# Kernel optimization log

Measured on AMD Instinct MI355X. Metric: run time of the kernel, lower is better.

Reference implementation:

```python
import jax, jax.numpy as jnp
import numpy as np

NUM_ITERS = 3
NUM_HEADS = 4
EPS = 1e-8
LN_EPS = 1e-5


def _layernorm(x, w, b):
    mu = jnp.mean(x, axis=-1, keepdims=True)
    var = jnp.mean(jnp.square(x - mu), axis=-1, keepdims=True)
    return (x - mu) * jax.lax.rsqrt(var + LN_EPS) * w + b


def setup_inputs() -> dict:
    key = jax.random.key(0)
    ks = jax.random.split(key, 12)
    B, K, D, Q, Hm = 64, 4096, 256, 8, 512
    s = 0.02
    return {
        "inputs": jax.random.normal(ks[0], (B, K, D), jnp.float32),
        "slots_init": jax.random.normal(ks[1], (B, Q, D), jnp.float32),
        "Wq": jax.random.normal(ks[2], (D, D), jnp.float32) * s,
        "Wk": jax.random.normal(ks[3], (D, D), jnp.float32) * s,
        "Wv": jax.random.normal(ks[4], (D, D), jnp.float32) * s,
        "ln_in_w": jnp.ones((D,), jnp.float32),
        "ln_in_b": jnp.zeros((D,), jnp.float32),
        "ln_slots_w": jnp.ones((D,), jnp.float32),
        "ln_slots_b": jnp.zeros((D,), jnp.float32),
        "ln_mlp_w": jnp.ones((D,), jnp.float32),
        "ln_mlp_b": jnp.zeros((D,), jnp.float32),
        "gru_Wih": jax.random.normal(ks[5], (3 * D, D), jnp.float32) * s,
        "gru_Whh": jax.random.normal(ks[6], (3 * D, D), jnp.float32) * s,
        "gru_bih": jnp.zeros((3 * D,), jnp.float32),
        "gru_bhh": jnp.zeros((3 * D,), jnp.float32),
        "mlp_W1": jax.random.normal(ks[7], (D, Hm), jnp.float32) * s,
        "mlp_b1": jnp.zeros((Hm,), jnp.float32),
        "mlp_W2": jax.random.normal(ks[8], (Hm, D), jnp.float32) * s,
        "mlp_b2": jnp.zeros((D,), jnp.float32),
    }


def reference(inputs, slots_init, Wq, Wk, Wv, ln_in_w, ln_in_b, ln_slots_w,
              ln_slots_b, ln_mlp_w, ln_mlp_b, gru_Wih, gru_Whh, gru_bih,
              gru_bhh, mlp_W1, mlp_b1, mlp_W2, mlp_b2):
    B, K, D = inputs.shape
    Q = slots_init.shape[1]
    H = NUM_HEADS
    dh = D // H
    scale = dh ** -0.5

    x = _layernorm(inputs, ln_in_w, ln_in_b)
    k = (x @ Wk).reshape(B, K, H, dh).transpose(0, 2, 1, 3) * scale  # [B,H,K,dh]
    v = (x @ Wv).reshape(B, K, H, dh).transpose(0, 2, 1, 3)          # [B,H,K,dh]

    slots = slots_init
    attn = None
    for _ in range(NUM_ITERS):
        slots_prev = slots
        s_n = _layernorm(slots, ln_slots_w, ln_slots_b)
        q = (s_n @ Wq).reshape(B, Q, H, dh).transpose(0, 2, 1, 3)    # [B,H,Q,dh]
        logits = jnp.einsum('bhkd,bhqd->bhkq', k, q)                 # [B,H,K,Q]
        # softmax jointly over (heads, slots) per kv position
        attn = jax.nn.softmax(
            logits.transpose(0, 2, 1, 3).reshape(B, K, H * Q), axis=-1
        ).reshape(B, K, H, Q).transpose(0, 2, 1, 3)                  # [B,H,K,Q]
        attn = attn + EPS
        attn = attn / jnp.sum(attn, axis=2, keepdims=True)           # renorm over K
        updates = jnp.einsum('bhkq,bhkd->bqhd', attn, v).reshape(B, Q, D)

        # GRU cell (PyTorch gate order: r, z, n)
        u = updates.reshape(-1, D)
        h = slots_prev.reshape(-1, D)
        gi = u @ gru_Wih.T + gru_bih
        gh = h @ gru_Whh.T + gru_bhh
        i_r, i_z, i_n = jnp.split(gi, 3, axis=-1)
        h_r, h_z, h_n = jnp.split(gh, 3, axis=-1)
        r = jax.nn.sigmoid(i_r + h_r)
        z = jax.nn.sigmoid(i_z + h_z)
        n = jnp.tanh(i_n + r * h_n)
        slots = ((1.0 - z) * n + z * h).reshape(B, Q, D)

        m = _layernorm(slots, ln_mlp_w, ln_mlp_b)
        slots = slots + jax.nn.relu(m @ mlp_W1 + mlp_b1) @ mlp_W2 + mlp_b2

    return slots, attn.mean(axis=1).transpose(0, 2, 1)  # [B,Q,D], [B,Q,K]
```

## Files before the change

kernel.cpp:

```cpp
#include <hip/hip_runtime.h>

#define B   64
#define KK  4096
#define D   256
#define Q   8
#define H   4
#define DH  64
#define HQ  32
#define HM  512
#define NCH 8
#define CHK 512
#define EPS 1e-8f
#define LNE 1e-5f
#define SCALE 0.125f

typedef short bf16x8 __attribute__((ext_vector_type(8)));
typedef float f32x4 __attribute__((ext_vector_type(4)));

__device__ __forceinline__ float bf2f(unsigned short u) {
    unsigned int x = ((unsigned int)u) << 16;
    float f; __builtin_memcpy(&f, &x, 4); return f;
}
__device__ __forceinline__ unsigned short f2bf(float f) {
    unsigned int x; __builtin_memcpy(&x, &f, 4);
    unsigned int lsb = (x >> 16) & 1u;
    x += 0x7fffu + lsb;
    return (unsigned short)(x >> 16);
}

__device__ __forceinline__ void gload16(const void* g, void* l) {
    __builtin_amdgcn_global_load_lds(
        (const __attribute__((address_space(1))) unsigned int*)g,
        (__attribute__((address_space(3))) unsigned int*)l, 16, 0, 0);
}

__device__ __forceinline__ void stage64x512B(const char* src, size_t row0,
                                             size_t stride, char* lds, int w, int l)
{
#pragma unroll
    for (int i = 0; i < 8; ++i) {
        const int seg = w * 8 + i;
        const int r = seg * 2 + (l >> 5);
        const int off = ((l & 31) * 16) ^ ((r & 7) << 4);
        gload16(src + (row0 + r) * stride + off, lds + seg * 1024);
    }
}

__global__ void k_init(const float* __restrict__ s0, float* __restrict__ slots,
                       unsigned short* __restrict__ slots_bf)
{
    const int i = blockIdx.x * 256 + threadIdx.x;
    const float v = s0[i];
    slots[i] = v; slots_bf[i] = f2bf(v);
}

__global__ __launch_bounds__(256) void k0_wkv(
    const float* __restrict__ Wk, const float* __restrict__ Wv,
    unsigned short* __restrict__ WkvT)
{
    const int c = blockIdx.x, d = threadIdx.x;
    const float v = (c < 256) ? Wk[(size_t)d * 256 + c] * SCALE
                              : Wv[(size_t)d * 256 + (c - 256)];
    WkvT[(size_t)c * 256 + d] = f2bf(v);
}

__global__ void k0_cvt(const float* __restrict__ src, unsigned short* __restrict__ dst)
{
    const int i = blockIdx.x * 256 + threadIdx.x;
    dst[i] = f2bf(src[i]);
}

__global__ void k0_t1(const float* __restrict__ W1, unsigned short* __restrict__ W1T)
{
    const int n = blockIdx.x, d = threadIdx.x;
    W1T[(size_t)n * 256 + d] = f2bf(W1[(size_t)d * 512 + n]);
}

__global__ void k0_t2(const float* __restrict__ W2, unsigned short* __restrict__ W2T)
{
    const int n = blockIdx.x, j = threadIdx.x;
    W2T[(size_t)n * 512 + j]       = f2bf(W2[(size_t)j * 256 + n]);
    W2T[(size_t)n * 512 + 256 + j] = f2bf(W2[(size_t)(256 + j) * 256 + n]);
}

__global__ __launch_bounds__(256) void k1_mfma(
    const float* __restrict__ inp, const unsigned short* __restrict__ WkvT,
    const float* __restrict__ lnw, const float* __restrict__ lnb,
    unsigned short* __restrict__ kbuf, unsigned short* __restrict__ vbufT)
{
    __shared__ char smem[65536];
    char* abase = smem;
    char* bb0 = smem + 32768;
    char* bb1 = smem;
    const int t = threadIdx.x, w = t >> 6, l = t & 63;
    const size_t row0 = (size_t)blockIdx.x * 64;

    float4 xv[16];
#pragma unroll
    for (int i = 0; i < 16; ++i)
        xv[i] = ((const float4*)(inp + (row0 + w * 16 + i) * D))[l];
    const float4 w4 = ((const float4*)lnw)[l];
    const float4 b4 = ((const float4*)lnb)[l];
#pragma unroll
    for (int i = 0; i < 16; ++i) {
        const int r = w * 16 + i;
        float4 x = xv[i];
        float s  = x.x + x.y + x.z + x.w;
        float ss = x.x*x.x + x.y*x.y + x.z*x.z + x.w*x.w;
#pragma unroll
        for (int off = 32; off; off >>= 1) { s += __shfl_xor(s, off); ss += __shfl_xor(ss, off); }
        const float mu = s * (1.f / 256.f);
        const float rs = rsqrtf(ss * (1.f / 256.f) - mu * mu + LNE);
        ushort4 pk;
        pk.x = f2bf((x.x - mu) * rs * w4.x + b4.x);
        pk.y = f2bf((x.y - mu) * rs * w4.y + b4.y);
        pk.z = f2bf((x.z - mu) * rs * w4.z + b4.z);
        pk.w = f2bf((x.w - mu) * rs * w4.w + b4.w);
        *(ushort4*)(abase + r * 512 + ((l * 8) ^ ((r & 7) << 4))) = pk;
    }
    __syncthreads();

    const int arow = w * 16 + (l & 15);
    const char* ap = abase + arow * 512;
    const int asw = (l & 7) << 4;
    bf16x8 af[8];
#pragma unroll
    for (int kk = 0; kk < 8; ++kk)
        af[kk] = *(const bf16x8*)(ap + ((kk * 64 + (l >> 4) * 16) ^ asw));

    stage64x512B((const char*)WkvT, 0, 512, bb0, w, l);
    __syncthreads();

    const f32x4 fz = {0.f, 0.f, 0.f, 0.f};
    for (int n2 = 0; n2 < 8; ++n2) {
        if (n2 < 7)
            stage64x512B((const char*)WkvT, (size_t)(n2 + 1) * 64, 512,
                         ((n2 + 1) & 1) ? bb1 : bb0, w, l);
        const char* bbase = (n2 & 1) ? bb1 : bb0;
        f32x4 acc[4] = {fz, fz, fz, fz};
#pragma unroll
        for (int kk = 0; kk < 8; ++kk) {
            const int koff = kk * 64 + (l >> 4) * 16;
#pragma unroll
            for (int nf = 0; nf < 4; ++nf) {
                const int brow = nf * 16 + (l & 15);
                const bf16x8 bf_ = *(const bf16x8*)(bbase + brow * 512 + (koff ^ ((brow & 7) << 4)));
                acc[nf] = __builtin_amdgcn_mfma_f32_16x16x32_bf16(af[kk], bf_, acc[nf], 0, 0, 0);
            }
        }
        const int c0 = n2 * 64;
        const size_t grow0 = row0 + w * 16 + (l >> 4) * 4;
#pragma unroll
        for (int nf = 0; nf < 4; ++nf) {
            const int c = c0 + nf * 16 + (l & 15);
            if (c < 256) {
#pragma unroll
                for (int reg = 0; reg < 4; ++reg)
                    kbuf[(grow0 + reg) * 256 + c] = f2bf(acc[nf][reg]);
            } else {
                const int cc = c - 256;
                const size_t bb = grow0 >> 12;
                const int kl = (int)(grow0 & 4095);
                ushort4 pk;
                pk.x = f2bf(acc[nf][0]); pk.y = f2bf(acc[nf][1]);
                pk.z = f2bf(acc[nf][2]); pk.w = f2bf(acc[nf][3]);
                *(ushort4*)(vbufT + ((bb * 256 + cc) * KK + kl)) = pk;
            }
        }
        __syncthreads();
    }
}

__global__ __launch_bounds__(256) void k2_qproj(
    const float* __restrict__ slots, const float* __restrict__ Wq,
    const float* __restrict__ lnw, const float* __restrict__ lnb, float* __restrict__ qbuf)
{
    const int row = blockIdx.x, t = threadIdx.x;
    __shared__ float sn[256];
    __shared__ float red[8];
    const float x = slots[(size_t)row * D + t];
    float mu, rs;
    {
        float s = x, ss = x * x;
#pragma unroll
        for (int off = 32; off; off >>= 1) { s += __shfl_xor(s, off); ss += __shfl_xor(ss, off); }
        if ((t & 63) == 0) { red[t >> 6] = s; red[4 + (t >> 6)] = ss; }
        __syncthreads();
        const float S  = red[0] + red[1] + red[2] + red[3];
        const float SS = red[4] + red[5] + red[6] + red[7];
        mu = S * (1.f / 256.f);
        rs = rsqrtf(SS * (1.f / 256.f) - mu * mu + LNE);
    }
    sn[t] = (x - mu) * rs * lnw[t] + lnb[t];
    __syncthreads();
    float acc = 0.f;
    for (int d = 0; d < 256; ++d) acc = fmaf(sn[d], Wq[(size_t)d * 256 + t], acc);
    qbuf[(size_t)row * D + t] = acc;
}

__global__ __launch_bounds__(256) void k_attn(
    const unsigned short* __restrict__ kbuf, const unsigned short* __restrict__ vbufT,
    const float* __restrict__ qbuf, float* __restrict__ updp,
    float* __restrict__ denp, float* __restrict__ pbuf, int write_p)
{
    __shared__ unsigned short ksm[64 * 256];
    __shared__ unsigned short vsm[256 * 64];
    __shared__ unsigned short psm[32 * 64];
    __shared__ float dred[4][32];
    const int t = threadIdx.x, w = t >> 6, l = t & 63;
    const int b = blockIdx.x >> 3, chunk = blockIdx.x & 7;
    const int k0g = chunk * CHK;
    const int n = l & 15, lg = l >> 4;

    auto stage_ks = [&](int tile) {
        const size_t rowg = (size_t)b * KK + k0g + tile * 64;
#pragma unroll
        for (int i = 0; i < 8; ++i) {
            const int seg = w * 8 + i;
            const int r = seg * 2 + (l >> 5);
            const int off = ((l & 31) * 16) ^ ((r & 7) << 4);
            gload16((const char*)kbuf + (rowg + r) * 512 + off, (char*)ksm + seg * 1024);
        }
    };
    auto stage_vs = [&](int tile) {
        const int kk0 = k0g + tile * 64;
#pragma unroll
        for (int i = 0; i < 8; ++i) {
            const int seg = w * 8 + i;
            const int d = seg * 8 + (l >> 3);
            const int off = ((l & 7) * 16) ^ ((d & 7) << 4);
            gload16((const char*)vbufT + (((size_t)b * 256 + d) * KK + kk0) * 2 + off,
                    (char*)vsm + seg * 1024);
        }
    };
    stage_ks(0); stage_vs(0);

    bf16x8 qf[2][2];
#pragma unroll
    for (int p = 0; p < 2; ++p) {
        const int h = p * 2 + (n >> 3);
        const float* qb = qbuf + ((size_t)b * Q + (n & 7)) * D;
#pragma unroll
        for (int j = 0; j < 2; ++j) {
            const int dbase = (h * 2 + j) * 32 + lg * 8;
            short tmp[8];
#pragma unroll
            for (int e = 0; e < 8; ++e) tmp[e] = (short)f2bf(qb[dbase + e]);
            __builtin_memcpy(&qf[p][j], tmp, 16);
        }
    }
    const bf16x8 ZV = {0,0,0,0,0,0,0,0};
    const f32x4 fz = {0.f,0.f,0.f,0.f};
    f32x4 pv[2][4];
#pragma unroll
    for (int mt = 0; mt < 2; ++mt)
#pragma unroll
        for (int nf = 0; nf < 4; ++nf) pv[mt][nf] = fz;
    float den0 = 0.f, den1 = 0.f;

    for (int tile = 0; tile < 8; ++tile) {
        __syncthreads();
        const int arow = w * 16 + n;
        const char* ap = (const char*)ksm + arow * 512;
        const int asw = (arow & 7) << 4;
        f32x4 lac[2] = {fz, fz};
#pragma unroll
        for (int kk = 0; kk < 8; ++kk) {
            const bf16x8 a = *(const bf16x8*)(ap + ((kk * 64 + lg * 16) ^ asw));
            const int p = kk >> 2;
            const bool on = (((kk & 3) >> 1) == (n >> 3));
            const bf16x8 bq = on ? qf[p][kk & 1] : ZV;
            if (p == 0) lac[0] = __builtin_amdgcn_mfma_f32_16x16x32_bf16(a, bq, lac[0], 0, 0, 0);
            else        lac[1] = __builtin_amdgcn_mfma_f32_16x16x32_bf16(a, bq, lac[1], 0, 0, 0);
        }
#pragma unroll
        for (int reg = 0; reg < 4; ++reg) {
            float m = fmaxf(lac[0][reg], lac[1][reg]);
#pragma unroll
            for (int off = 8; off; off >>= 1) m = fmaxf(m, __shfl_xor(m, off));
            const float e0 = __expf(lac[0][reg] - m);
            const float e1 = __expf(lac[1][reg] - m);
            float se = e0 + e1;
#pragma unroll
            for (int off = 8; off; off >>= 1) se += __shfl_xor(se, off);
            const float inv = 1.f / se;
            lac[0][reg] = e0 * inv; lac[1][reg] = e1 * inv;
            den0 += lac[0][reg];    den1 += lac[1][reg];
        }
        const int kb = w * 16 + lg * 4;
        {
            ushort4 p0, p1;
            p0.x = f2bf(lac[0][0]); p0.y = f2bf(lac[0][1]); p0.z = f2bf(lac[0][2]); p0.w = f2bf(lac[0][3]);
            p1.x = f2bf(lac[1][0]); p1.y = f2bf(lac[1][1]); p1.z = f2bf(lac[1][2]); p1.w = f2bf(lac[1][3]);
            *(ushort4*)((char*)psm + n * 128 + ((kb * 2) ^ ((n & 7) << 4))) = p0;
            *(ushort4*)((char*)psm + (16 + n) * 128 + ((kb * 2) ^ ((n & 7) << 4))) = p1;
        }
        if (write_p) {
            float* pp = pbuf + ((size_t)b * KK + k0g + tile * 64 + kb) * HQ;
#pragma unroll
            for (int reg = 0; reg < 4; ++reg) {
                pp[(size_t)reg * HQ + n] = lac[0][reg];
                pp[(size_t)reg * HQ + 16 + n] = lac[1][reg];
            }
        }
        __syncthreads();
        if (tile < 7) stage_ks(tile + 1);
#pragma unroll
        for (int kk = 0; kk < 2; ++kk) {
            const int koff = kk * 64 + lg * 16;
            const bf16x8 a0 = *(const bf16x8*)((char*)psm + n * 128 + (koff ^ ((n & 7) << 4)));
            const bf16x8 a1 = *(const bf16x8*)((char*)psm + (16 + n) * 128 + (koff ^ ((n & 7) << 4)));
#pragma unroll
            for (int nf = 0; nf < 4; ++nf) {
                const int d = w * 64 + nf * 16 + n;
                const bf16x8 bv = *(const bf16x8*)((char*)vsm + d * 128 + (koff ^ ((d & 7) << 4)));
                pv[0][nf] = __builtin_amdgcn_mfma_f32_16x16x32_bf16(a0, bv, pv[0][nf], 0, 0, 0);
                pv[1][nf] = __builtin_amdgcn_mfma_f32_16x16x32_bf16(a1, bv, pv[1][nf], 0, 0, 0);
            }
        }
        __syncthreads();
        if (tile < 7) stage_vs(tile + 1);
    }

    den0 += __shfl_xor(den0, 16); den0 += __shfl_xor(den0, 32);
    den1 += __shfl_xor(den1, 16); den1 += __shfl_xor(den1, 32);
    if (l < 16) { dred[w][l] = den0; dred[w][16 + l] = den1; }
    __syncthreads();
    if (t < 32)
        denp[((size_t)b * NCH + chunk) * HQ + t] =
            dred[0][t] + dred[1][t] + dred[2][t] + dred[3][t];

    if ((lg >> 1) == (w & 1)) {
        const int mt = w >> 1;
#pragma unroll
        for (int nf = 0; nf < 4; ++nf) {
#pragma unroll
            for (int reg = 0; reg < 4; ++reg) {
                const int q = (lg & 1) * 4 + reg;
                updp[(((size_t)b * NCH + chunk) * Q + q) * D + w * 64 + nf * 16 + n] = pv[mt][nf][reg];
            }
        }
    }
}

__global__ __launch_bounds__(256) void k_reduce(
    const float* __restrict__ updp, const float* __restrict__ denp,
    unsigned short* __restrict__ updbf)
{
    const int row = blockIdx.x, t = threadIdx.x;
    const int b = row >> 3, q = row & 7, h = t >> 6;
    float ds = 0.f, us = 0.f;
#pragma unroll
    for (int c = 0; c < NCH; ++c) {
        ds += denp[((size_t)b * NCH + c) * HQ + h * Q + q];
        us += updp[(((size_t)b * NCH + c) * Q + q) * D + t];
    }
    updbf[(size_t)row * D + t] = f2bf(us / (ds + (float)KK * EPS));
}

__global__ void k_den(const float* __restrict__ denp, float* __restrict__ invden)
{
    const int b = blockIdx.x, t = threadIdx.x;
    float s = 0.f;
#pragma unroll
    for (int c = 0; c < NCH; ++c) s += denp[((size_t)b * NCH + c) * HQ + t];
    invden[b * HQ + t] = 1.f / (s + (float)KK * EPS);
}

__global__ __launch_bounds__(256) void k_gru(
    const unsigned short* __restrict__ updbf, const unsigned short* __restrict__ slotsbf,
    const unsigned short* __restrict__ Wihbf, const unsigned short* __restrict__ Whhbf,
    float* __restrict__ gg)
{
    __shared__ unsigned short As[64 * 256];
    __shared__ unsigned short Bs[64 * 256];
    const int t = threadIdx.x, w = t >> 6, l = t & 63;
    const int rb = blockIdx.x / 24, nb = blockIdx.x % 24;
    const unsigned short* Asrc = (nb < 12) ? updbf : slotsbf;
    stage64x512B((const char*)Asrc, (size_t)rb * 64, 512, (char*)As, w, l);
    if (nb < 12) stage64x512B((const char*)Wihbf, (size_t)nb * 64, 512, (char*)Bs, w, l);
    else         stage64x512B((const char*)Whhbf, (size_t)(nb - 12) * 64, 512, (char*)Bs, w, l);
    __syncthreads();
    const int arow = w * 16 + (l & 15);
    const int asw = (l & 7) << 4;
    bf16x8 af[8];
#pragma unroll
    for (int kk = 0; kk < 8; ++kk)
        af[kk] = *(const bf16x8*)((char*)As + arow * 512 + ((kk * 64 + (l >> 4) * 16) ^ asw));
    const f32x4 fz = {0.f,0.f,0.f,0.f};
    f32x4 acc[4] = {fz, fz, fz, fz};
#pragma unroll
    for (int kk = 0; kk < 8; ++kk) {
        const int koff = kk * 64 + (l >> 4) * 16;
#pragma unroll
        for (int nf = 0; nf < 4; ++nf) {
            const int brow = nf * 16 + (l & 15);
            const bf16x8 bf_ = *(const bf16x8*)((char*)Bs + brow * 512 + (koff ^ ((brow & 7) << 4)));
            acc[nf] = __builtin_amdgcn_mfma_f32_16x16x32_bf16(af[kk], bf_, acc[nf], 0, 0, 0);
        }
    }
    const int colbase = (nb < 12) ? nb * 64 : 768 + (nb - 12) * 64;
#pragma unroll
    for (int nf = 0; nf < 4; ++nf) {
        const int col = colbase + nf * 16 + (l & 15);
#pragma unroll
        for (int reg = 0; reg < 4; ++reg) {
            const size_t row = (size_t)rb * 64 + w * 16 + (l >> 4) * 4 + reg;
            gg[row * 1536 + col] = acc[nf][reg];
        }
    }
}

__global__ __launch_bounds__(256) void k_gates(
    const float* __restrict__ gg, const float* __restrict__ slots,
    const float* __restrict__ bih, const float* __restrict__ bhh,
    const float* __restrict__ lnw, const float* __restrict__ lnb,
    float* __restrict__ snew, unsigned short* __restrict__ mbf)
{
    const int row = blockIdx.x, t = threadIdx.x;
    __shared__ float red[8];
    const float* g = gg + (size_t)row * 1536;
    const float i_r = g[t]        + bih[t];
    const float i_z = g[256 + t]  + bih[256 + t];
    const float i_n = g[512 + t]  + bih[512 + t];
    const float h_r = g[768 + t]  + bhh[t];
    const float h_z = g[1024 + t] + bhh[256 + t];
    const float h_n = g[1280 + t] + bhh[512 + t];
    const float r = 1.f / (1.f + __expf(-(i_r + h_r)));
    const float z = 1.f / (1.f + __expf(-(i_z + h_z)));
    const float nn = tanhf(i_n + r * h_n);
    const float h0 = slots[(size_t)row * D + t];
    const float sn = (1.f - z) * nn + z * h0;
    snew[(size_t)row * D + t] = sn;
    float mu, rs;
    {
        float s = sn, ss = sn * sn;
#pragma unroll
        for (int off = 32; off; off >>= 1) { s += __shfl_xor(s, off); ss += __shfl_xor(ss, off); }
        if ((t & 63) == 0) { red[t >> 6] = s; red[4 + (t >> 6)] = ss; }
        __syncthreads();
        const float S  = red[0] + red[1] + red[2] + red[3];
        const float SS = red[4] + red[5] + red[6] + red[7];
        mu = S * (1.f / 256.f);
        rs = rsqrtf(SS * (1.f / 256.f) - mu * mu + LNE);
    }
    mbf[(size_t)row * D + t] = f2bf((sn - mu) * rs * lnw[t] + lnb[t]);
}

__global__ __launch_bounds__(256) void k_mlp1(
    const unsigned short* __restrict__ mbf, const unsigned short* __restrict__ W1T,
    const float* __restrict__ b1, unsigned short* __restrict__ hidbf)
{
    __shared__ unsigned short As[64 * 256];
    __shared__ unsigned short Bs[64 * 256];
    const int t = threadIdx.x, w = t >> 6, l = t & 63;
    const int rb = blockIdx.x >> 3, nb = blockIdx.x & 7;
    stage64x512B((const char*)mbf, (size_t)rb * 64, 512, (char*)As, w, l);
    stage64x512B((const char*)W1T, (size_t)nb * 64, 512, (char*)Bs, w, l);
    __syncthreads();
    const int arow = w * 16 + (l & 15);
    const int asw = (l & 7) << 4;
    bf16x8 af[8];
#pragma unroll
    for (int kk = 0; kk < 8; ++kk)
        af[kk] = *(const bf16x8*)((char*)As + arow * 512 + ((kk * 64 + (l >> 4) * 16) ^ asw));
    const f32x4 fz = {0.f,0.f,0.f,0.f};
    f32x4 acc[4] = {fz, fz, fz, fz};
#pragma unroll
    for (int kk = 0; kk < 8; ++kk) {
        const int koff = kk * 64 + (l >> 4) * 16;
#pragma unroll
        for (int nf = 0; nf < 4; ++nf) {
            const int brow = nf * 16 + (l & 15);
            const bf16x8 bf_ = *(const bf16x8*)((char*)Bs + brow * 512 + (koff ^ ((brow & 7) << 4)));
            acc[nf] = __builtin_amdgcn_mfma_f32_16x16x32_bf16(af[kk], bf_, acc[nf], 0, 0, 0);
        }
    }
#pragma unroll
    for (int nf = 0; nf < 4; ++nf) {
        const int col = nb * 64 + nf * 16 + (l & 15);
        const float bb = b1[col];
#pragma unroll
        for (int reg = 0; reg < 4; ++reg) {
            const size_t row = (size_t)rb * 64 + w * 16 + (l >> 4) * 4 + reg;
            hidbf[row * HM + col] = f2bf(fmaxf(acc[nf][reg] + bb, 0.f));
        }
    }
}

__global__ __launch_bounds__(256) void k_mlp2(
    const unsigned short* __restrict__ hidbf, const unsigned short* __restrict__ W2T,
    const float* __restrict__ b2, const float* __restrict__ snew,
    float* __restrict__ slots, unsigned short* __restrict__ slotsbf)
{
    __shared__ unsigned short As[64 * 256];
    __shared__ unsigned short Bs[64 * 256];
    const int t = threadIdx.x, w = t >> 6, l = t & 63;
    const int rb = blockIdx.x >> 2, nb = blockIdx.x & 3;
    const f32x4 fz = {0.f,0.f,0.f,0.f};
    f32x4 acc[4] = {fz, fz, fz, fz};
    for (int c = 0; c < 2; ++c) {
        stage64x512B((const char*)hidbf + c * 512, (size_t)rb * 64, 1024, (char*)As, w, l);
        stage64x512B((const char*)W2T + c * 512, (size_t)nb * 64, 1024, (char*)Bs, w, l);
        __syncthreads();
        const int arow = w * 16 + (l & 15);
        const int asw = (l & 7) << 4;
        bf16x8 af[8];
#pragma unroll
        for (int kk = 0; kk < 8; ++kk)
            af[kk] = *(const bf16x8*)((char*)As + arow * 512 + ((kk * 64 + (l >> 4) * 16) ^ asw));
#pragma unroll
        for (int kk = 0; kk < 8; ++kk) {
            const int koff = kk * 64 + (l >> 4) * 16;
#pragma unroll
            for (int nf = 0; nf < 4; ++nf) {
                const int brow = nf * 16 + (l & 15);
                const bf16x8 bf_ = *(const bf16x8*)((char*)Bs + brow * 512 + (koff ^ ((brow & 7) << 4)));
                acc[nf] = __builtin_amdgcn_mfma_f32_16x16x32_bf16(af[kk], bf_, acc[nf], 0, 0, 0);
            }
        }
        __syncthreads();
    }
#pragma unroll
    for (int nf = 0; nf < 4; ++nf) {
        const int col = nb * 64 + nf * 16 + (l & 15);
        const float bb = b2[col];
#pragma unroll
        for (int reg = 0; reg < 4; ++reg) {
            const size_t row = (size_t)rb * 64 + w * 16 + (l >> 4) * 4 + reg;
            const float v = snew[row * D + col] + acc[nf][reg] + bb;
            slots[row * D + col] = v;
            slotsbf[row * D + col] = f2bf(v);
        }
    }
}

__global__ void k7_copy(const float* __restrict__ s, float* __restrict__ o)
{
    const int i = blockIdx.x * 256 + threadIdx.x;
    o[i] = s[i];
}

__global__ __launch_bounds__(256) void k7_attnout(
    const float* __restrict__ pbuf, const float* __restrict__ invden, float* __restrict__ out2)
{
    const int blk = blockIdx.x;
    const int b = blk >> 4;
    const int kk0 = (blk & 15) * 256;
    __shared__ float ps[256][33];
    __shared__ float inv[32];
    const int t = threadIdx.x;
    const float* pp = pbuf + ((size_t)b * KK + kk0) * HQ;
    for (int i = 0; i < 32; ++i) {
        const int idx = i * 256 + t;
        ps[idx >> 5][idx & 31] = pp[idx];
    }
    if (t < 32) inv[t] = invden[b * HQ + t];
    __syncthreads();
    float* o = out2 + (size_t)b * Q * KK + kk0 + t;
#pragma unroll
    for (int q = 0; q < 8; ++q) {
        float v = 0.f;
#pragma unroll
        for (int hh = 0; hh < 4; ++hh)
            v += (ps[t][hh * 8 + q] + EPS) * inv[hh * 8 + q];
        o[(size_t)q * KK] = v * 0.25f;
    }
}

extern "C" void kernel_launch(void* const* d_in, const int* in_sizes, int n_in,
                              void* d_out, int out_size, void* d_ws, size_t ws_size,
                              hipStream_t stream)
{
    const float* inputs  = (const float*)d_in[0];
    const float* slots0  = (const float*)d_in[1];
    const float* Wq      = (const float*)d_in[2];
    const float* Wk      = (const float*)d_in[3];
    const float* Wv      = (const float*)d_in[4];
    const float* ln_in_w = (const float*)d_in[5];
    const float* ln_in_b = (const float*)d_in[6];
    const float* ln_s_w  = (const float*)d_in[7];
    const float* ln_s_b  = (const float*)d_in[8];
    const float* ln_m_w  = (const float*)d_in[9];
    const float* ln_m_b  = (const float*)d_in[10];
    const float* gWih    = (const float*)d_in[11];
    const float* gWhh    = (const float*)d_in[12];
    const float* gbih    = (const float*)d_in[13];
    const float* gbhh    = (const float*)d_in[14];
    const float* W1      = (const float*)d_in[15];
    const float* b1      = (const float*)d_in[16];
    const float* W2      = (const float*)d_in[17];
    const float* b2      = (const float*)d_in[18];

    char* p = (char*)d_ws;
    unsigned short* kbuf  = (unsigned short*)p; p += (size_t)B * KK * D * 2;
    unsigned short* vbufT = (unsigned short*)p; p += (size_t)B * KK * D * 2;
    float* pbuf   = (float*)p; p += (size_t)B * KK * HQ * 4;
    float* updp   = (float*)p; p += (size_t)B * NCH * Q * D * 4;
    float* denp   = (float*)p; p += (size_t)B * NCH * HQ * 4;
    float* invden = (float*)p; p += (size_t)B * HQ * 4;
    float* qbuf   = (float*)p; p += (size_t)B * Q * D * 4;
    float* slots  = (float*)p; p += (size_t)B * Q * D * 4;
    float* snew   = (float*)p; p += (size_t)B * Q * D * 4;
    unsigned short* slots_bf = (unsigned short*)p; p += (size_t)B * Q * D * 2;
    unsigned short* upd_bf   = (unsigned short*)p; p += (size_t)B * Q * D * 2;
    unsigned short* mbf      = (unsigned short*)p; p += (size_t)B * Q * D * 2;
    unsigned short* hidbf    = (unsigned short*)p; p += (size_t)B * Q * HM * 2;
    unsigned short* WkvT     = (unsigned short*)p; p += (size_t)512 * 256 * 2;
    unsigned short* Wihbf    = (unsigned short*)p; p += (size_t)768 * 256 * 2;
    unsigned short* Whhbf    = (unsigned short*)p; p += (size_t)768 * 256 * 2;
    unsigned short* W1T      = (unsigned short*)p; p += (size_t)HM * 256 * 2;
    unsigned short* W2T      = (unsigned short*)p; p += (size_t)256 * HM * 2;
    float* gg = updp;

    k_init<<<(B * Q * D) / 256, 256, 0, stream>>>(slots0, slots, slots_bf);
    k0_wkv<<<512, 256, 0, stream>>>(Wk, Wv, WkvT);
    k0_cvt<<<768, 256, 0, stream>>>(gWih, Wihbf);
    k0_cvt<<<768, 256, 0, stream>>>(gWhh, Whhbf);
    k0_t1<<<512, 256, 0, stream>>>(W1, W1T);
    k0_t2<<<256, 256, 0, stream>>>(W2, W2T);
    k1_mfma<<<(B * KK) / 64, 256, 0, stream>>>(inputs, WkvT, ln_in_w, ln_in_b, kbuf, vbufT);
    for (int it = 0; it < 3; ++it) {
        k2_qproj<<<B * Q, 256, 0, stream>>>(slots, Wq, ln_s_w, ln_s_b, qbuf);
        k_attn<<<B * NCH, 256, 0, stream>>>(kbuf, vbufT, qbuf, updp, denp, pbuf, (it == 2) ? 1 : 0);
        k_reduce<<<B * Q, 256, 0, stream>>>(updp, denp, upd_bf);
        k_gru<<<8 * 24, 256, 0, stream>>>(upd_bf, slots_bf, Wihbf, Whhbf, gg);
        k_gates<<<B * Q, 256, 0, stream>>>(gg, slots, gbih, gbhh, ln_m_w, ln_m_b, snew, mbf);
        k_mlp1<<<8 * 8, 256, 0, stream>>>(mbf, W1T, b1, hidbf);
        k_mlp2<<<8 * 4, 256, 0, stream>>>(hidbf, W2T, b2, snew, slots, slots_bf);
    }
    k_den<<<B, 32, 0, stream>>>(denp, invden);
    k7_copy<<<(B * Q * D) / 256, 256, 0, stream>>>(slots, (float*)d_out);
    k7_attnout<<<B * (KK / 256), 256, 0, stream>>>(pbuf, invden, (float*)d_out + (size_t)B * Q * D);
}
```

Measured before the change: 464.2 us.

## Fold input LayerNorm into KV projection, pre-pack K/V fragments, fuse prep kernels

Applies the input LayerNorm algebraically after the K/V GEMM using precomputed column sums of the ln-weighted projection, so raw inputs are converted straight to bf16. K and V are written in MFMA-fragment-packed tiles, so the attention kernel stages them with contiguous loads and reads fragments without swizzle math. Softmax max-subtraction is removed, the weight-prep kernels are merged into one launch, and the final slots copy and denominator kernel are folded into mlp2 and attnout. Dropping the max and normalizing after rounding raw x to bf16 carry numerical-range and precision risk.

```diff
diff --git a/kernel.cpp b/kernel.cpp
--- a/kernel.cpp
+++ b/kernel.cpp
@@ -17,6 +17,8 @@
 typedef short bf16x8 __attribute__((ext_vector_type(8)));
 typedef float f32x4 __attribute__((ext_vector_type(4)));
 
+#define MFMA __builtin_amdgcn_mfma_f32_16x16x32_bf16
+
 __device__ __forceinline__ float bf2f(unsigned short u) {
     unsigned int x = ((unsigned int)u) << 16;
     float f; __builtin_memcpy(&f, &x, 4); return f;
@@ -46,79 +48,105 @@
     }
 }
 
-__global__ void k_init(const float* __restrict__ s0, float* __restrict__ slots,
-                       unsigned short* __restrict__ slots_bf)
-{
-    const int i = blockIdx.x * 256 + threadIdx.x;
-    const float v = s0[i];
-    slots[i] = v; slots_bf[i] = f2bf(v);
-}
-
-__global__ __launch_bounds__(256) void k0_wkv(
+__global__ __launch_bounds__(256) void k_prep(
     const float* __restrict__ Wk, const float* __restrict__ Wv,
-    unsigned short* __restrict__ WkvT)
-{
-    const int c = blockIdx.x, d = threadIdx.x;
-    const float v = (c < 256) ? Wk[(size_t)d * 256 + c] * SCALE
-                              : Wv[(size_t)d * 256 + (c - 256)];
-    WkvT[(size_t)c * 256 + d] = f2bf(v);
-}
-
-__global__ void k0_cvt(const float* __restrict__ src, unsigned short* __restrict__ dst)
-{
-    const int i = blockIdx.x * 256 + threadIdx.x;
-    dst[i] = f2bf(src[i]);
-}
-
-__global__ void k0_t1(const float* __restrict__ W1, unsigned short* __restrict__ W1T)
-{
-    const int n = blockIdx.x, d = threadIdx.x;
-    W1T[(size_t)n * 256 + d] = f2bf(W1[(size_t)d * 512 + n]);
-}
-
-__global__ void k0_t2(const float* __restrict__ W2, unsigned short* __restrict__ W2T)
-{
-    const int n = blockIdx.x, j = threadIdx.x;
-    W2T[(size_t)n * 512 + j]       = f2bf(W2[(size_t)j * 256 + n]);
-    W2T[(size_t)n * 512 + 256 + j] = f2bf(W2[(size_t)(256 + j) * 256 + n]);
+    const float* __restrict__ lnw, const float* __restrict__ lnb,
+    const float* __restrict__ gWih, const float* __restrict__ gWhh,
+    const float* __restrict__ W1, const float* __restrict__ W2,
+    const float* __restrict__ Wq, const float* __restrict__ s0,
+    unsigned short* __restrict__ wpk, float* __restrict__ cs, float* __restrict__ b2v,
+    unsigned short* __restrict__ Wihbf, unsigned short* __restrict__ Whhbf,
+    unsigned short* __restrict__ W1T, unsigned short* __restrict__ W2T,
+    float* __restrict__ slots, unsigned short* __restrict__ slots_bf)
+{
+    const int blk = blockIdx.x, t = threadIdx.x;
+    if (blk < 256) {
+        const int ct = blk >> 3, kt = blk & 7;
+#pragma unroll
+        for (int e2 = 0; e2 < 2; ++e2) {
+            const int i = t * 2 + e2;
+            const int lane = i >> 3, e = i & 7;
+            const int col = ct * 16 + (lane & 15);
+            const int k = kt * 32 + (lane >> 4) * 8 + e;
+            const float wv = lnw[k];
+            const float v = (col < 256) ? wv * Wk[(size_t)k * 256 + col] * SCALE
+                                        : wv * Wv[(size_t)k * 256 + (col - 256)];
+            wpk[(size_t)blk * 512 + i] = f2bf(v);
+        }
+    } else if (blk < 258) {
+        const int c = (blk - 256) * 256 + t;
+        float s1 = 0.f, s2 = 0.f;
+        for (int k = 0; k < 256; ++k) {
+            const float wraw = (c < 256) ? Wk[(size_t)k * 256 + c] * SCALE
+                                         : Wv[(size_t)k * 256 + (c - 256)];
+            s1 += lnw[k] * wraw;
+            s2 += lnb[k] * wraw;
+        }
+        cs[c] = s1; b2v[c] = s2;
+    } else if (blk < 1026) {
+        const int i = (blk - 258) * 256 + t;
+        Wihbf[i] = f2bf(gWih[i]);
+    } else if (blk < 1794) {
+        const int i = (blk - 1026) * 256 + t;
+        Whhbf[i] = f2bf(gWhh[i]);
+    } else if (blk < 2306) {
+        const int nn = blk - 1794;
+        W1T[(size_t)nn * 256 + t] = f2bf(W1[(size_t)t * 512 + nn]);
+    } else if (blk < 2562) {
+        const int nn = blk - 2306;
+        W2T[(size_t)nn * 512 + t]       = f2bf(W2[(size_t)t * 256 + nn]);
+        W2T[(size_t)nn * 512 + 256 + t] = f2bf(W2[(size_t)(256 + t) * 256 + nn]);
+    } else {
+        const int i = (blk - 2562) * 256 + t;
+        const float v = s0[i];
+        slots[i] = v; slots_bf[i] = f2bf(v);
+    }
 }
 
 __global__ __launch_bounds__(256) void k1_mfma(
-    const float* __restrict__ inp, const unsigned short* __restrict__ WkvT,
-    const float* __restrict__ lnw, const float* __restrict__ lnb,
-    unsigned short* __restrict__ kbuf, unsigned short* __restrict__ vbufT)
-{
-    __shared__ char smem[65536];
+    const float* __restrict__ inp, const unsigned short* __restrict__ wpk,
+    const float* __restrict__ cs, const float* __restrict__ b2v,
+    unsigned short* __restrict__ kpk, unsigned short* __restrict__ vpk)
+{
+    __shared__ char smem[32768];
     char* abase = smem;
-    char* bb0 = smem + 32768;
-    char* bb1 = smem;
+    char* bb0 = smem;
+    char* bb1 = smem + 16384;
     const int t = threadIdx.x, w = t >> 6, l = t & 63;
     const size_t row0 = (size_t)blockIdx.x * 64;
+    const int b_blk = blockIdx.x >> 6;
+    const int kbase = (blockIdx.x & 63) * 64;
+    const int lg = l >> 4;
+
+    auto stageB = [&](int n2, char* dst) {
+#pragma unroll
+        for (int i = 0; i < 4; ++i) {
+            const int seg = w * 4 + i;
+            gload16((const char*)wpk + (size_t)n2 * 16384 + seg * 1024 + l * 16,
+                    dst + seg * 1024);
+        }
+    };
 
     float4 xv[16];
 #pragma unroll
     for (int i = 0; i < 16; ++i)
         xv[i] = ((const float4*)(inp + (row0 + w * 16 + i) * D))[l];
-    const float4 w4 = ((const float4*)lnw)[l];
-    const float4 b4 = ((const float4*)lnb)[l];
+    float rsA = 0.f, muA = 0.f;
 #pragma unroll
     for (int i = 0; i < 16; ++i) {
         const int r = w * 16 + i;
-        float4 x = xv[i];
+        const float4 x = xv[i];
         float s  = x.x + x.y + x.z + x.w;
         float ss = x.x*x.x + x.y*x.y + x.z*x.z + x.w*x.w;
 #pragma unroll
         for (int off = 32; off; off >>= 1) { s += __shfl_xor(s, off); ss += __shfl_xor(ss, off); }
         const float mu = s * (1.f / 256.f);
         const float rs = rsqrtf(ss * (1.f / 256.f) - mu * mu + LNE);
+        if ((l & 15) == i) { rsA = rs; muA = rs * mu; }
         ushort4 pk;
-        pk.x = f2bf((x.x - mu) * rs * w4.x + b4.x);
-        pk.y = f2bf((x.y - mu) * rs * w4.y + b4.y);
-        pk.z = f2bf((x.z - mu) * rs * w4.z + b4.z);
-        pk.w = f2bf((x.w - mu) * rs * w4.w + b4.w);
+        pk.x = f2bf(x.x); pk.y = f2bf(x.y); pk.z = f2bf(x.z); pk.w = f2bf(x.w);
         *(ushort4*)(abase + r * 512 + ((l * 8) ^ ((r & 7) << 4))) = pk;
     }
-    __syncthreads();
 
     const int arow = w * 16 + (l & 15);
     const char* ap = abase + arow * 512;
@@ -126,48 +154,72 @@
     bf16x8 af[8];
 #pragma unroll
     for (int kk = 0; kk < 8; ++kk)
-        af[kk] = *(const bf16x8*)(ap + ((kk * 64 + (l >> 4) * 16) ^ asw));
-
-    stage64x512B((const char*)WkvT, 0, 512, bb0, w, l);
+        af[kk] = *(const bf16x8*)(ap + ((kk * 64 + lg * 16) ^ asw));
+    float rsV[4], muV[4];
+#pragma unroll
+    for (int r = 0; r < 4; ++r) {
+        rsV[r] = __shfl(rsA, lg * 4 + r);
+        muV[r] = __shfl(muA, lg * 4 + r);
+    }
     __syncthreads();
+    stageB(0, bb0); stageB(1, bb1);
+    __syncthreads();
 
     const f32x4 fz = {0.f, 0.f, 0.f, 0.f};
-    for (int n2 = 0; n2 < 8; ++n2) {
-        if (n2 < 7)
-            stage64x512B((const char*)WkvT, (size_t)(n2 + 1) * 64, 512,
-                         ((n2 + 1) & 1) ? bb1 : bb0, w, l);
+    for (int n2 = 0; n2 < 16; ++n2) {
         const char* bbase = (n2 & 1) ? bb1 : bb0;
-        f32x4 acc[4] = {fz, fz, fz, fz};
-#pragma unroll
-        for (int kk = 0; kk < 8; ++kk) {
-            const int koff = kk * 64 + (l >> 4) * 16;
-#pragma unroll
-            for (int nf = 0; nf < 4; ++nf) {
-                const int brow = nf * 16 + (l & 15);
-                const bf16x8 bf_ = *(const bf16x8*)(bbase + brow * 512 + (koff ^ ((brow & 7) << 4)));
-                acc[nf] = __builtin_amdgcn_mfma_f32_16x16x32_bf16(af[kk], bf_, acc[nf], 0, 0, 0);
-            }
-        }
-        const int c0 = n2 * 64;
-        const size_t grow0 = row0 + w * 16 + (l >> 4) * 4;
-#pragma unroll
-        for (int nf = 0; nf < 4; ++nf) {
-            const int c = c0 + nf * 16 + (l & 15);
-            if (c < 256) {
-#pragma unroll
-                for (int reg = 0; reg < 4; ++reg)
-                    kbuf[(grow0 + reg) * 256 + c] = f2bf(acc[nf][reg]);
-            } else {
-                const int cc = c - 256;
-                const size_t bb = grow0 >> 12;
-                const int kl = (int)(grow0 & 4095);
+        f32x4 acc[2] = {fz, fz};
+        if (n2 < 8) {
+#pragma unroll
+            for (int kk = 0; kk < 8; ++kk) {
+                const bf16x8 b0 = *(const bf16x8*)(bbase + kk * 1024 + l * 16);
+                const bf16x8 b1 = *(const bf16x8*)(bbase + 8192 + kk * 1024 + l * 16);
+                acc[0] = MFMA(b0, af[kk], acc[0], 0, 0, 0);
+                acc[1] = MFMA(b1, af[kk], acc[1], 0, 0, 0);
+            }
+            const int kt16 = (kbase >> 4) + w;
+#pragma unroll
+            for (int nf = 0; nf < 2; ++nf) {
+                const int d0 = n2 * 32 + nf * 16 + lg * 4;
+                const float4 cs4 = *(const float4*)(cs + d0);
+                const float4 bb4 = *(const float4*)(b2v + d0);
+                unsigned short* kp = kpk
+                    + ((((size_t)b_blk * 256 + kt16) * 8 + n2) * 512)
+                    + ((l & 15) + ((nf * 2 + (lg >> 1)) << 4)) * 8 + (lg & 1) * 4;
                 ushort4 pk;
-                pk.x = f2bf(acc[nf][0]); pk.y = f2bf(acc[nf][1]);
-                pk.z = f2bf(acc[nf][2]); pk.w = f2bf(acc[nf][3]);
-                *(ushort4*)(vbufT + ((bb * 256 + cc) * KK + kl)) = pk;
-            }
-        }
-        __syncthreads();
+                pk.x = f2bf(rsA * acc[nf][0] - muA * cs4.x + bb4.x);
+                pk.y = f2bf(rsA * acc[nf][1] - muA * cs4.y + bb4.y);
+                pk.z = f2bf(rsA * acc[nf][2] - muA * cs4.z + bb4.z);
+                pk.w = f2bf(rsA * acc[nf][3] - muA * cs4.w + bb4.w);
+                *(ushort4*)kp = pk;
+            }
+        } else {
+#pragma unroll
+            for (int kk = 0; kk < 8; ++kk) {
+                const bf16x8 b0 = *(const bf16x8*)(bbase + kk * 1024 + l * 16);
+                const bf16x8 b1 = *(const bf16x8*)(bbase + 8192 + kk * 1024 + l * 16);
+                acc[0] = MFMA(af[kk], b0, acc[0], 0, 0, 0);
+                acc[1] = MFMA(af[kk], b1, acc[1], 0, 0, 0);
+            }
+            const int kt32 = (kbase >> 5) + (w >> 1);
+#pragma unroll
+            for (int nf = 0; nf < 2; ++nf) {
+                const int c = n2 * 32 + nf * 16 + (l & 15);
+                const float csc = cs[c], b2c = b2v[c];
+                const int dt16 = (n2 - 8) * 2 + nf;
+                unsigned short* vp = vpk
+                    + ((((size_t)b_blk * 128 + kt32) * 16 + dt16) * 512)
+                    + ((l & 15) + (((w & 1) * 2 + (lg >> 1)) << 4)) * 8 + (lg & 1) * 4;
+                ushort4 pk;
+                pk.x = f2bf(rsV[0] * acc[nf][0] - muV[0] * csc + b2c);
+                pk.y = f2bf(rsV[1] * acc[nf][1] - muV[1] * csc + b2c);
+                pk.z = f2bf(rsV[2] * acc[nf][2] - muV[2] * csc + b2c);
+                pk.w = f2bf(rsV[3] * acc[nf][3] - muV[3] * csc + b2c);
+                *(ushort4*)vp = pk;
+            }
+        }
+        __syncthreads();
+        if (n2 < 14) stageB(n2 + 2, (n2 & 1) ? bb1 : bb0);
     }
 }
 
@@ -199,13 +251,13 @@
 }
 
 __global__ __launch_bounds__(256) void k_attn(
-    const unsigned short* __restrict__ kbuf, const unsigned short* __restrict__ vbufT,
+    const unsigned short* __restrict__ kpk, const unsigned short* __restrict__ vpk,
     const float* __restrict__ qbuf, float* __restrict__ updp,
     float* __restrict__ denp, float* __restrict__ pbuf, int write_p)
 {
     __shared__ unsigned short ksm[64 * 256];
-    __shared__ unsigned short vsm[256 * 64];
-    __shared__ unsigned short psm[32 * 64];
+    __shared__ unsigned short vsm[64 * 256];
+    __shared__ unsigned short psm[2048];
     __shared__ float dred[4][32];
     const int t = threadIdx.x, w = t >> 6, l = t & 63;
     const int b = blockIdx.x >> 3, chunk = blockIdx.x & 7;
@@ -213,24 +265,21 @@
     const int n = l & 15, lg = l >> 4;
 
     auto stage_ks = [&](int tile) {
-        const size_t rowg = (size_t)b * KK + k0g + tile * 64;
+        const char* src = (const char*)kpk
+            + (((size_t)b * 256 + chunk * 32 + tile * 4) * 8) * 1024 + l * 16;
 #pragma unroll
         for (int i = 0; i < 8; ++i) {
             const int seg = w * 8 + i;
-            const int r = seg * 2 + (l >> 5);
-            const int off = ((l & 31) * 16) ^ ((r & 7) << 4);
-            gload16((const char*)kbuf + (rowg + r) * 512 + off, (char*)ksm + seg * 1024);
+            gload16(src + seg * 1024, (char*)ksm + seg * 1024);
         }
     };
     auto stage_vs = [&](int tile) {
-        const int kk0 = k0g + tile * 64;
+        const char* src = (const char*)vpk
+            + (((size_t)b * 128 + chunk * 16 + tile * 2) * 16) * 1024 + l * 16;
 #pragma unroll
         for (int i = 0; i < 8; ++i) {
             const int seg = w * 8 + i;
-            const int d = seg * 8 + (l >> 3);
-            const int off = ((l & 7) * 16) ^ ((d & 7) << 4);
-            gload16((const char*)vbufT + (((size_t)b * 256 + d) * KK + kk0) * 2 + off,
-                    (char*)vsm + seg * 1024);
+            gload16(src + seg * 1024, (char*)vsm + seg * 1024);
         }
     };
     stage_ks(0); stage_vs(0);
@@ -260,26 +309,20 @@
 
     for (int tile = 0; tile < 8; ++tile) {
         __syncthreads();
-        const int arow = w * 16 + n;
-        const char* ap = (const char*)ksm + arow * 512;
-        const int asw = (arow & 7) << 4;
         f32x4 lac[2] = {fz, fz};
 #pragma unroll
         for (int kk = 0; kk < 8; ++kk) {
-            const bf16x8 a = *(const bf16x8*)(ap + ((kk * 64 + lg * 16) ^ asw));
+            const bf16x8 kf = *(const bf16x8*)((char*)ksm + (w * 8 + kk) * 1024 + l * 16);
             const int p = kk >> 2;
             const bool on = (((kk & 3) >> 1) == (n >> 3));
             const bf16x8 bq = on ? qf[p][kk & 1] : ZV;
-            if (p == 0) lac[0] = __builtin_amdgcn_mfma_f32_16x16x32_bf16(a, bq, lac[0], 0, 0, 0);
-            else        lac[1] = __builtin_amdgcn_mfma_f32_16x16x32_bf16(a, bq, lac[1], 0, 0, 0);
+            if (p == 0) lac[0] = MFMA(kf, bq, lac[0], 0, 0, 0);
+            else        lac[1] = MFMA(kf, bq, lac[1], 0, 0, 0);
         }
 #pragma unroll
         for (int reg = 0; reg < 4; ++reg) {
-            float m = fmaxf(lac[0][reg], lac[1][reg]);
-#pragma unroll
-            for (int off = 8; off; off >>= 1) m = fmaxf(m, __shfl_xor(m, off));
-            const float e0 = __expf(lac[0][reg] - m);
-            const float e1 = __expf(lac[1][reg] - m);
+            const float e0 = __expf(lac[0][reg]);
+            const float e1 = __expf(lac[1][reg]);
             float se = e0 + e1;
 #pragma unroll
             for (int off = 8; off; off >>= 1) se += __shfl_xor(se, off);
@@ -287,13 +330,14 @@
             lac[0][reg] = e0 * inv; lac[1][reg] = e1 * inv;
             den0 += lac[0][reg];    den1 += lac[1][reg];
         }
+        char* pb = (char*)psm;
         const int kb = w * 16 + lg * 4;
         {
             ushort4 p0, p1;
             p0.x = f2bf(lac[0][0]); p0.y = f2bf(lac[0][1]); p0.z = f2bf(lac[0][2]); p0.w = f2bf(lac[0][3]);
             p1.x = f2bf(lac[1][0]); p1.y = f2bf(lac[1][1]); p1.z = f2bf(lac[1][2]); p1.w = f2bf(lac[1][3]);
-            *(ushort4*)((char*)psm + n * 128 + ((kb * 2) ^ ((n & 7) << 4))) = p0;
-            *(ushort4*)((char*)psm + (16 + n) * 128 + ((kb * 2) ^ ((n & 7) << 4))) = p1;
+            *(ushort4*)(pb + n * 128 + ((kb * 2) ^ ((n & 7) << 4))) = p0;
+            *(ushort4*)(pb + (16 + n) * 128 + ((kb * 2) ^ ((n & 7) << 4))) = p1;
         }
         if (write_p) {
             float* pp = pbuf + ((size_t)b * KK + k0g + tile * 64 + kb) * HQ;
@@ -306,16 +350,15 @@
         __syncthreads();
         if (tile < 7) stage_ks(tile + 1);
 #pragma unroll
-        for (int kk = 0; kk < 2; ++kk) {
-            const int koff = kk * 64 + lg * 16;
-            const bf16x8 a0 = *(const bf16x8*)((char*)psm + n * 128 + (koff ^ ((n & 7) << 4)));
-            const bf16x8 a1 = *(const bf16x8*)((char*)psm + (16 + n) * 128 + (koff ^ ((n & 7) << 4)));
+        for (int kkp = 0; kkp < 2; ++kkp) {
+            const int koff = kkp * 64 + lg * 16;
+            const bf16x8 a0 = *(const bf16x8*)(pb + n * 128 + (koff ^ ((n & 7) << 4)));
+            const bf16x8 a1 = *(const bf16x8*)(pb + (16 + n) * 128 + (koff ^ ((n & 7) << 4)));
 #pragma unroll
             for (int nf = 0; nf < 4; ++nf) {
-                const int d = w * 64 + nf * 16 + n;
-                const bf16x8 bv = *(const bf16x8*)((char*)vsm + d * 128 + (koff ^ ((d & 7) << 4)));
-                pv[0][nf] = __builtin_amdgcn_mfma_f32_16x16x32_bf16(a0, bv, pv[0][nf], 0, 0, 0);
-                pv[1][nf] = __builtin_amdgcn_mfma_f32_16x16x32_bf16(a1, bv, pv[1][nf], 0, 0, 0);
+                const bf16x8 bv = *(const bf16x8*)((char*)vsm + (kkp * 16 + w * 4 + nf) * 1024 + l * 16);
+                pv[0][nf] = MFMA(a0, bv, pv[0][nf], 0, 0, 0);
+                pv[1][nf] = MFMA(a1, bv, pv[1][nf], 0, 0, 0);
             }
         }
         __syncthreads();
@@ -356,15 +399,6 @@
         us += updp[(((size_t)b * NCH + c) * Q + q) * D + t];
     }
     updbf[(size_t)row * D + t] = f2bf(us / (ds + (float)KK * EPS));
-}
-
-__global__ void k_den(const float* __restrict__ denp, float* __restrict__ invden)
-{
-    const int b = blockIdx.x, t = threadIdx.x;
-    float s = 0.f;
-#pragma unroll
-    for (int c = 0; c < NCH; ++c) s += denp[((size_t)b * NCH + c) * HQ + t];
-    invden[b * HQ + t] = 1.f / (s + (float)KK * EPS);
 }
 
 __global__ __launch_bounds__(256) void k_gru(
@@ -396,7 +430,7 @@
         for (int nf = 0; nf < 4; ++nf) {
             const int brow = nf * 16 + (l & 15);
             const bf16x8 bf_ = *(const bf16x8*)((char*)Bs + brow * 512 + (koff ^ ((brow & 7) << 4)));
-            acc[nf] = __builtin_amdgcn_mfma_f32_16x16x32_bf16(af[kk], bf_, acc[nf], 0, 0, 0);
+            acc[nf] = MFMA(af[kk], bf_, acc[nf], 0, 0, 0);
         }
     }
     const int colbase = (nb < 12) ? nb * 64 : 768 + (nb - 12) * 64;
@@ -473,7 +507,7 @@
         for (int nf = 0; nf < 4; ++nf) {
             const int brow = nf * 16 + (l & 15);
             const bf16x8 bf_ = *(const bf16x8*)((char*)Bs + brow * 512 + (koff ^ ((brow & 7) << 4)));
-            acc[nf] = __builtin_amdgcn_mfma_f32_16x16x32_bf16(af[kk], bf_, acc[nf], 0, 0, 0);
+            acc[nf] = MFMA(af[kk], bf_, acc[nf], 0, 0, 0);
         }
     }
 #pragma unroll
@@ -491,7 +525,8 @@
 __global__ __launch_bounds__(256) void k_mlp2(
     const unsigned short* __restrict__ hidbf, const unsigned short* __restrict__ W2T,
     const float* __restrict__ b2, const float* __restrict__ snew,
-    float* __restrict__ slots, unsigned short* __restrict__ slotsbf)
+    float* __restrict__ slots, unsigned short* __restrict__ slotsbf,
+    float* __restrict__ outp)
 {
     __shared__ unsigned short As[64 * 256];
     __shared__ unsigned short Bs[64 * 256];
@@ -516,7 +551,7 @@
             for (int nf = 0; nf < 4; ++nf) {
                 const int brow = nf * 16 + (l & 15);
                 const bf16x8 bf_ = *(const bf16x8*)((char*)Bs + brow * 512 + (koff ^ ((brow & 7) << 4)));
-                acc[nf] = __builtin_amdgcn_mfma_f32_16x16x32_bf16(af[kk], bf_, acc[nf], 0, 0, 0);
+                acc[nf] = MFMA(af[kk], bf_, acc[nf], 0, 0, 0);
             }
         }
         __syncthreads();
@@ -531,18 +566,13 @@
             const float v = snew[row * D + col] + acc[nf][reg] + bb;
             slots[row * D + col] = v;
             slotsbf[row * D + col] = f2bf(v);
-        }
-    }
-}
-
-__global__ void k7_copy(const float* __restrict__ s, float* __restrict__ o)
-{
-    const int i = blockIdx.x * 256 + threadIdx.x;
-    o[i] = s[i];
+            if (outp) outp[row * D + col] = v;
+        }
+    }
 }
 
 __global__ __launch_bounds__(256) void k7_attnout(
-    const float* __restrict__ pbuf, const float* __restrict__ invden, float* __restrict__ out2)
+    const float* __restrict__ pbuf, const float* __restrict__ denp, float* __restrict__ out2)
 {
     const int blk = blockIdx.x;
     const int b = blk >> 4;
@@ -555,7 +585,12 @@
         const int idx = i * 256 + t;
         ps[idx >> 5][idx & 31] = pp[idx];
     }
-    if (t < 32) inv[t] = invden[b * HQ + t];
+    if (t < 32) {
+        float s = 0.f;
+#pragma unroll
+        for (int c = 0; c < NCH; ++c) s += denp[((size_t)b * NCH + c) * HQ + t];
+        inv[t] = 1.f / (s + (float)KK * EPS);
+    }
     __syncthreads();
     float* o = out2 + (size_t)b * Q * KK + kk0 + t;
 #pragma unroll
@@ -593,12 +628,11 @@
     const float* b2      = (const float*)d_in[18];
 
     char* p = (char*)d_ws;
-    unsigned short* kbuf  = (unsigned short*)p; p += (size_t)B * KK * D * 2;
-    unsigned short* vbufT = (unsigned short*)p; p += (size_t)B * KK * D * 2;
+    unsigned short* kpk   = (unsigned short*)p; p += (size_t)B * KK * D * 2;
+    unsigned short* vpk   = (unsigned short*)p; p += (size_t)B * KK * D * 2;
     float* pbuf   = (float*)p; p += (size_t)B * KK * HQ * 4;
     float* updp   = (float*)p; p += (size_t)B * NCH * Q * D * 4;
     float* denp   = (float*)p; p += (size_t)B * NCH * HQ * 4;
-    float* invden = (float*)p; p += (size_t)B * HQ * 4;
     float* qbuf   = (float*)p; p += (size_t)B * Q * D * 4;
     float* slots  = (float*)p; p += (size_t)B * Q * D * 4;
     float* snew   = (float*)p; p += (size_t)B * Q * D * 4;
@@ -606,30 +640,29 @@
     unsigned short* upd_bf   = (unsigned short*)p; p += (size_t)B * Q * D * 2;
     unsigned short* mbf      = (unsigned short*)p; p += (size_t)B * Q * D * 2;
     unsigned short* hidbf    = (unsigned short*)p; p += (size_t)B * Q * HM * 2;
-    unsigned short* WkvT     = (unsigned short*)p; p += (size_t)512 * 256 * 2;
-    unsigned short* Wihbf    = (unsigned short*)p; p += (size_t)768 * 256 * 2;
-    unsigned short* Whhbf    = (unsigned short*)p; p += (size_t)768 * 256 * 2;
-    unsigned short* W1T      = (unsigned short*)p; p += (size_t)HM * 256 * 2;
-    unsigned short* W2T      = (unsigned short*)p; p += (size_t)256 * HM * 2;
+    unsigned short* wpk   = (unsigned short*)p; p += (size_t)512 * 256 * 2;
+    float* csv    = (float*)p; p += 512 * 4;
+    float* b2vv   = (float*)p; p += 512 * 4;
+    unsigned short* Wihbf = (unsigned short*)p; p += (size_t)768 * 256 * 2;
+    unsigned short* Whhbf = (unsigned short*)p; p += (size_t)768 * 256 * 2;
+    unsigned short* W1T   = (unsigned short*)p; p += (size_t)HM * 256 * 2;
+    unsigned short* W2T   = (unsigned short*)p; p += (size_t)256 * HM * 2;
     float* gg = updp;
 
-    k_init<<<(B * Q * D) / 256, 256, 0, stream>>>(slots0, slots, slots_bf);
-    k0_wkv<<<512, 256, 0, stream>>>(Wk, Wv, WkvT);
-    k0_cvt<<<768, 256, 0, stream>>>(gWih, Wihbf);
-    k0_cvt<<<768, 256, 0, stream>>>(gWhh, Whhbf);
-    k0_t1<<<512, 256, 0, stream>>>(W1, W1T);
-    k0_t2<<<256, 256, 0, stream>>>(W2, W2T);
-    k1_mfma<<<(B * KK) / 64, 256, 0, stream>>>(inputs, WkvT, ln_in_w, ln_in_b, kbuf, vbufT);
+    k_prep<<<3074, 256, 0, stream>>>(Wk, Wv, ln_in_w, ln_in_b, gWih, gWhh, W1, W2, Wq, slots0,
+                                     wpk, csv, b2vv, Wihbf, Whhbf, W1T, W2T, slots, slots_bf);
+    k1_mfma<<<(B * KK) / 64, 256, 0, stream>>>(inputs, wpk, csv, b2vv, kpk, vpk);
+    k2_qproj<<<B * Q, 256, 0, stream>>>(slots, Wq, ln_s_w, ln_s_b, qbuf);
     for (int it = 0; it < 3; ++it) {
-        k2_qproj<<<B * Q, 256, 0, stream>>>(slots, Wq, ln_s_w, ln_s_b, qbuf);
-        k_attn<<<B * NCH, 256, 0, stream>>>(kbuf, vbufT, qbuf, updp, denp, pbuf, (it == 2) ? 1 : 0);
+        k_attn<<<B * NCH, 256, 0, stream>>>(kpk, vpk, qbuf, updp, denp, pbuf, (it == 2) ? 1 : 0);
         k_reduce<<<B * Q, 256, 0, stream>>>(updp, denp, upd_bf);
         k_gru<<<8 * 24, 256, 0, stream>>>(upd_bf, slots_bf, Wihbf, Whhbf, gg);
         k_gates<<<B * Q, 256, 0, stream>>>(gg, slots, gbih, gbhh, ln_m_w, ln_m_b, snew, mbf);
         k_mlp1<<<8 * 8, 256, 0, stream>>>(mbf, W1T, b1, hidbf);
-        k_mlp2<<<8 * 4, 256, 0, stream>>>(hidbf, W2T, b2, snew, slots, slots_bf);
-    }
-    k_den<<<B, 32, 0, stream>>>(denp, invden);
-    k7_copy<<<(B * Q * D) / 256, 256, 0, stream>>>(slots, (float*)d_out);
-    k7_attnout<<<B * (KK / 256), 256, 0, stream>>>(pbuf, invden, (float*)d_out + (size_t)B * Q * D);
-}
+        k_mlp2<<<8 * 4, 256, 0, stream>>>(hidbf, W2T, b2, snew, slots, slots_bf,
+                                          (it == 2) ? (float*)d_out : (float*)nullptr);
+        if (it < 2)
+            k2_qproj<<<B * Q, 256, 0, stream>>>(slots, Wq, ln_s_w, ln_s_b, qbuf);
+    }
+    k7_attnout<<<B * (KK / 256), 256, 0, stream>>>(pbuf, denp, (float*)d_out + (size_t)B * Q * D);
+}
```

After: 500.4 us. 7.8% more time.
